# Kernel tuning notes

Hardware: AMD Instinct MI355X
Metric: run time of the kernel (lower is better)

## Reference

```python
import jax, jax.numpy as jnp
import numpy as np


def setup_inputs() -> dict:
    key = jax.random.key(0)
    ks = jax.random.split(key, 7)
    C, IC, H, W, B = 512, 256, 64, 64, 8
    N = H * W
    return {
        "x": jax.random.normal(ks[0], (B, C, H, W), dtype=jnp.float32),
        "w_phi": jax.random.normal(ks[1], (IC, C), dtype=jnp.float32) * 0.02,
        "w_theta": jax.random.normal(ks[2], (IC, C), dtype=jnp.float32) * 0.02,
        "w_g": jax.random.normal(ks[3], (IC, C), dtype=jnp.float32) * 0.02,
        "w_mask": jax.random.normal(ks[4], (C, IC), dtype=jnp.float32) * 0.02,
        "pos_embedding": jax.random.normal(ks[5], (1, N, N), dtype=jnp.float32),
        "pos_embedding_decoder": jax.random.normal(ks[6], (1, IC, H, W), dtype=jnp.float32),
    }


def reference(x, w_phi, w_theta, w_g, w_mask, pos_embedding, pos_embedding_decoder):
    b, c, h, w = x.shape
    n = h * w
    xf = x.reshape(b, c, n)  # [b, c, n]
    # 1x1 convs as channel matmuls
    phi = jnp.einsum('oc,bcn->bon', w_phi, xf)      # [b, ic, n]
    theta = jnp.einsum('oc,bcn->bon', w_theta, xf)  # [b, ic, n]
    g = jnp.einsum('oc,bcn->bon', w_g, xf) + pos_embedding_decoder.reshape(1, -1, n)
    g = jnp.swapaxes(g, 1, 2)  # [b, n, ic]
    # attention logits: theta^T @ phi -> [b, n_theta, n_phi], plus learned pos bias
    attn = jnp.einsum('bci,bcj->bij', theta, phi) + pos_embedding
    # NOTE: original softmax is over dim=1 (the theta/query axis), non-standard
    attn = jax.nn.softmax(attn, axis=1)
    y = jnp.einsum('bij,bjc->bic', attn, g)  # [b, n, ic]
    y = jnp.swapaxes(y, 1, 2).reshape(b, -1, n)  # [b, ic, n]
    mask = jnp.einsum('oc,bcn->bon', w_mask, y).reshape(b, c, h, w)
    return mask + x
```

## Files before the change

kernel.cpp:

```cpp
#include <hip/hip_runtime.h>

typedef short bf8 __attribute__((ext_vector_type(8)));
typedef float f32x4 __attribute__((ext_vector_type(4)));
typedef unsigned short us4 __attribute__((ext_vector_type(4)));
typedef unsigned short us8 __attribute__((ext_vector_type(8)));

#define DEVI __device__ __forceinline__

constexpr int NB = 8, NC = 512, NIC = 256, NS = 4096;

constexpr size_t OFF_XT  = 0;
constexpr size_t OFF_TP  = 33554432;
constexpr size_t OFF_POS = 67108864;
constexpr size_t OFF_G   = 100663296;
constexpr size_t OFF_RS  = 117440512;
constexpr size_t OFF_Y   = 134217728;
constexpr size_t OFF_WTP = 150994944;
constexpr size_t OFF_WG  = 151519232;
constexpr size_t OFF_WM  = 151781376;
constexpr size_t OFF_SP  = 152043520;

DEVI unsigned short f2bf(float f){
  unsigned u = __float_as_uint(f);
  u += 0x7fffu + ((u >> 16) & 1u);
  return (unsigned short)(u >> 16);
}
DEVI float bf2f(unsigned short b){ return __uint_as_float(((unsigned)b) << 16); }

DEVI void gld16(const void* g, void* l){
  __builtin_amdgcn_global_load_lds((const __attribute__((address_space(1))) unsigned int*)g,
                                   (__attribute__((address_space(3))) unsigned int*)l, 16, 0, 0);
}

DEVI void stageT(unsigned short* dst, const unsigned short* src, int ld, int wid, int lane){
  int rl = lane >> 3;
  int ce = ((lane & 7) << 3) ^ (rl << 3);
#pragma unroll
  for (int it = 0; it < 4; ++it){
    int q = wid + it * 4;
    gld16(src + (size_t)(q * 8 + rl) * ld + ce, dst + q * 512);
  }
}

DEVI void zero44(f32x4 (&a)[4][4]){
  f32x4 z = {0.f, 0.f, 0.f, 0.f};
#pragma unroll
  for (int i = 0; i < 4; ++i)
#pragma unroll
    for (int j = 0; j < 4; ++j) a[i][j] = z;
}

template<int NK64>
DEVI void gemm128v(const unsigned short* Ag, int lda, const unsigned short* Bg, int ldb,
                   unsigned short (&As)[2][8192], unsigned short (&Bs)[2][8192],
                   f32x4 (&acc)[4][4], int wid, int lane)
{
  const int wr = wid >> 1, wc = wid & 1;
  stageT(As[0], Ag, lda, wid, lane);
  stageT(Bs[0], Bg, ldb, wid, lane);
  __syncthreads();
  for (int kt = 0; kt < NK64; ++kt){
    int cur = kt & 1;
    if (kt + 1 < NK64){
      stageT(As[cur ^ 1], Ag + (kt + 1) * 64, lda, wid, lane);
      stageT(Bs[cur ^ 1], Bg + (kt + 1) * 64, ldb, wid, lane);
    }
    bf8 a[2][4], b[2][4];
#pragma unroll
    for (int ks = 0; ks < 2; ++ks){
      int cb = ks * 64 + ((lane >> 4) << 4);
#pragma unroll
      for (int f = 0; f < 4; ++f){
        int rA = wr * 64 + f * 16 + (lane & 15);
        a[ks][f] = *(const bf8*)((char*)As[cur] + rA * 128 + (cb ^ ((rA & 7) << 4)));
        int rB = wc * 64 + f * 16 + (lane & 15);
        b[ks][f] = *(const bf8*)((char*)Bs[cur] + rB * 128 + (cb ^ ((rB & 7) << 4)));
      }
    }
    __builtin_amdgcn_s_setprio(1);
#pragma unroll
    for (int ks = 0; ks < 2; ++ks)
#pragma unroll
      for (int i = 0; i < 4; ++i)
#pragma unroll
        for (int j = 0; j < 4; ++j)
          acc[i][j] = __builtin_amdgcn_mfma_f32_16x16x32_bf16(a[ks][i], b[ks][j], acc[i][j], 0, 0, 0);
    __builtin_amdgcn_s_setprio(0);
    __syncthreads();
  }
}


__global__ void k_prep(const float* wphi, const float* wtheta, const float* wgf, const float* wmf,
                       unsigned short* wtp, unsigned short* wgb, unsigned short* wmb){
  int idx = (blockIdx.x * 256 + threadIdx.x) * 4;
  const float* src; unsigned short* dst;
  if (idx < 131072)      { src = wphi + idx;            dst = wtp + idx; }
  else if (idx < 262144) { src = wtheta + (idx - 131072); dst = wtp + idx; }
  else if (idx < 393216) { src = wgf + (idx - 262144);  dst = wgb + (idx - 262144); }
  else                   { src = wmf + (idx - 393216);  dst = wmb + (idx - 393216); }
  f32x4 v = *(const f32x4*)src;
  us4 o;
#pragma unroll
  for (int r = 0; r < 4; ++r) o[r] = f2bf(v[r]);
  *(us4*)dst = o;
}

__global__ void k_pos(const float* pos, unsigned short* posb){
  size_t base = ((size_t)blockIdx.x * 256 + threadIdx.x) * 8;
  f32x4 v0 = *(const f32x4*)&pos[base];
  f32x4 v1 = *(const f32x4*)&pos[base + 4];
  us8 o;
#pragma unroll
  for (int r = 0; r < 4; ++r){ o[r] = f2bf(v0[r]); o[r + 4] = f2bf(v1[r]); }
  *(us8*)&posb[base] = o;
}

__global__ void k_xt(const float* x, unsigned short* xT){
  int b = blockIdx.z, ct = blockIdx.y, nt = blockIdx.x;
  __shared__ float t[64][65];
  int tid = threadIdx.x;
  int c0 = ct * 64, n0 = nt * 64;
  const float* xp = x + (size_t)b * NC * NS;
#pragma unroll
  for (int it = 0; it < 16; ++it){
    int idx = it * 256 + tid; int r = idx >> 6, cc = idx & 63;
    t[r][cc] = xp[(size_t)(c0 + r) * NS + n0 + cc];
  }
  __syncthreads();
  unsigned short* xo = xT + (size_t)b * NS * NC;
#pragma unroll
  for (int it = 0; it < 16; ++it){
    int idx = it * 256 + tid; int r = idx >> 6, cc = idx & 63;
    xo[(size_t)(n0 + r) * NC + c0 + cc] = f2bf(t[cc][r]);
  }
}


__global__ __launch_bounds__(256, 2) void k_tp(const unsigned short* wtp, const unsigned short* xT,
                                               unsigned short* tp){
  int b = blockIdx.z, ot = blockIdx.y, nt = blockIdx.x;
  int tid = threadIdx.x, wid = tid >> 6, lane = tid & 63, wr = wid >> 1, wc = wid & 1;
  __shared__ unsigned short As[2][8192], Bs[2][8192];
  f32x4 acc[4][4]; zero44(acc);
  gemm128v<8>(wtp + (size_t)(ot * 128) * 512, 512,
              xT + ((size_t)b * NS + nt * 128) * 512, 512, As, Bs, acc, wid, lane);
  unsigned short* out = tp + (size_t)b * NS * 512;
#pragma unroll
  for (int fr = 0; fr < 4; ++fr)
#pragma unroll
    for (int fc = 0; fc < 4; ++fc){
      int o0 = ot * 128 + wr * 64 + fr * 16 + ((lane >> 4) << 2);
      int n  = nt * 128 + wc * 64 + fc * 16 + (lane & 15);
      us4 v;
#pragma unroll
      for (int r = 0; r < 4; ++r) v[r] = f2bf(acc[fr][fc][r]);
      *(us4*)&out[(size_t)n * 512 + o0] = v;
    }
}

__global__ __launch_bounds__(256, 2) void k_g(const unsigned short* xT, const unsigned short* wgb,
                                              const float* pdec, unsigned short* gb){
  int b = blockIdx.z, ot = blockIdx.y, nt = blockIdx.x;
  int tid = threadIdx.x, wid = tid >> 6, lane = tid & 63, wr = wid >> 1, wc = wid & 1;
  __shared__ unsigned short As[2][8192], Bs[2][8192];
  f32x4 acc[4][4]; zero44(acc);
  gemm128v<8>(xT + ((size_t)b * NS + nt * 128) * 512, 512,
              wgb + (size_t)(ot * 128) * 512, 512, As, Bs, acc, wid, lane);
#pragma unroll
  for (int fr = 0; fr < 4; ++fr)
#pragma unroll
    for (int fc = 0; fc < 4; ++fc){
      int n0 = nt * 128 + wr * 64 + fr * 16 + ((lane >> 4) << 2);
      int o  = ot * 128 + wc * 64 + fc * 16 + (lane & 15);
      f32x4 pd = *(const f32x4*)&pdec[(size_t)o * NS + n0];
      us4 v;
#pragma unroll
      for (int r = 0; r < 4; ++r) v[r] = f2bf(acc[fr][fc][r] + pd[r]);
      *(us4*)&gb[((size_t)b * NIC + o) * NS + n0] = v;
    }
}

__global__ __launch_bounds__(256, 2) void k_stats(const unsigned short* tp, const unsigned short* posb,
                                                  float* sp){
  int b = blockIdx.z, ih = blockIdx.y, jt = blockIdx.x;
  int tid = threadIdx.x, wid = tid >> 6, lane = tid & 63, wr = wid >> 1, wc = wid & 1;
  __shared__ unsigned short As[2][8192], Bs[2][8192];
  __shared__ float sred[2][2][64];
  float sacc[4][4];
#pragma unroll
  for (int i = 0; i < 4; ++i)
#pragma unroll
    for (int j = 0; j < 4; ++j) sacc[i][j] = 0.f;
  const unsigned short* tpb = tp + (size_t)b * NS * 512;
  const unsigned short* Ag = tpb + (size_t)(jt * 128) * 512;
  for (int it8 = 0; it8 < 8; ++it8){
    int i0 = (ih * 8 + it8) * 128;
    const unsigned short* Bg = tpb + (size_t)i0 * 512 + 256;
    f32x4 acc[4][4]; zero44(acc);
    gemm128v<4>(Ag, 512, Bg, 512, As, Bs, acc, wid, lane);
#pragma unroll
    for (int fr = 0; fr < 4; ++fr)
#pragma unroll
      for (int fc = 0; fc < 4; ++fc){
        int ig  = i0 + wc * 64 + fc * 16 + (lane & 15);
        int jg0 = jt * 128 + wr * 64 + fr * 16 + ((lane >> 4) << 2);
        us4 pv = *(const us4*)&posb[(size_t)ig * NS + jg0];
#pragma unroll
        for (int r = 0; r < 4; ++r)
          sacc[fr][r] += __expf(acc[fr][fc][r] + bf2f(pv[r]));
      }
  }
#pragma unroll
  for (int m = 1; m <= 8; m <<= 1)
#pragma unroll
    for (int fr = 0; fr < 4; ++fr)
#pragma unroll
      for (int r = 0; r < 4; ++r)
        sacc[fr][r] += __shfl_xor(sacc[fr][r], m, 64);
  if ((lane & 15) == 0){
#pragma unroll
    for (int fr = 0; fr < 4; ++fr)
#pragma unroll
      for (int r = 0; r < 4; ++r)
        sred[wr][wc][fr * 16 + ((lane >> 4) << 2) + r] = sacc[fr][r];
  }
  __syncthreads();
  if (tid < 128){
    int jl = tid;
    sp[((size_t)b * 4 + ih) * NS + jt * 128 + jl] = sred[jl >> 6][0][jl & 63] + sred[jl >> 6][1][jl & 63];
  }
}

__global__ void k_rs(const float* sp, float* rs){
  int idx = blockIdx.x * 256 + threadIdx.x;
  int b = idx >> 12, j = idx & 4095;
  const float* spb = sp + (size_t)b * 4 * NS + j;
  rs[idx] = 1.f / (spb[0] + spb[NS] + spb[2 * NS] + spb[3 * NS]);
}

__global__ __launch_bounds__(256, 2) void k_y(const unsigned short* tp, const unsigned short* posb,
                                              const unsigned short* gb, const float* rs,
                                              unsigned short* yb){
  int b = blockIdx.y, i0 = blockIdx.x * 64;
  int tid = threadIdx.x, wid = tid >> 6, lane = tid & 63;
  __shared__ unsigned short Th[64 * 256];
  __shared__ unsigned short Aph[2][128 * 64];
  __shared__ unsigned short El[64 * 128];
  const unsigned short* tpb = tp + (size_t)b * NS * 512;

#pragma unroll
  for (int t = 0; t < 8; ++t){
    int cid = t * 256 + tid;
    int row = cid >> 5, ch = cid & 31;
    int dstb = row * 512 + ((ch * 16) ^ ((row & 7) << 4));
    *(us8*)((char*)Th + dstb) = *(const us8*)&tpb[(size_t)(i0 + row) * 512 + 256 + ch * 8];
  }
  f32x4 yacc[4][4]; zero44(yacc);
  stageT(Aph[0], tpb, 512, wid, lane);
  __syncthreads();

  const unsigned short* gbb = gb + (size_t)b * NIC * NS;
  const float* rsb = rs + (size_t)b * NS;

  for (int jt = 0; jt < 32; ++jt){
    int j0 = jt * 128;
    const unsigned short* phiBase = tpb + (size_t)j0 * 512;
    f32x4 lacc[2][4];
    {
      f32x4 z = {0.f, 0.f, 0.f, 0.f};
#pragma unroll
      for (int i = 0; i < 2; ++i)
#pragma unroll
        for (int j = 0; j < 4; ++j) lacc[i][j] = z;
    }
#pragma unroll
    for (int ph = 0; ph < 4; ++ph){
      int cur = ph & 1;
      if (ph < 3) stageT(Aph[cur ^ 1], phiBase + (ph + 1) * 64, 512, wid, lane);
      bf8 a[2][2], bt[2][4];
#pragma unroll
      for (int ks = 0; ks < 2; ++ks){
#pragma unroll
        for (int f = 0; f < 2; ++f){
          int r = wid * 32 + f * 16 + (lane & 15);
          int lb = ks * 64 + ((lane >> 4) << 4);
          a[ks][f] = *(const bf8*)((char*)Aph[cur] + r * 128 + (lb ^ ((r & 7) << 4)));
        }
#pragma unroll
        for (int f = 0; f < 4; ++f){
          int ti = f * 16 + (lane & 15);
          int tb = ph * 128 + ks * 64 + ((lane >> 4) << 4);
          bt[ks][f] = *(const bf8*)((char*)Th + ti * 512 + (tb ^ ((ti & 7) << 4)));
        }
      }
      __builtin_amdgcn_s_setprio(1);
#pragma unroll
      for (int ks = 0; ks < 2; ++ks)
#pragma unroll
        for (int fr = 0; fr < 2; ++fr)
#pragma unroll
          for (int fc = 0; fc < 4; ++fc)
            lacc[fr][fc] = __builtin_amdgcn_mfma_f32_16x16x32_bf16(a[ks][fr], bt[ks][fc], lacc[fr][fc], 0, 0, 0);
      __builtin_amdgcn_s_setprio(0);
      if (ph < 3) __syncthreads();
    }
#pragma unroll
    for (int fr = 0; fr < 2; ++fr)
#pragma unroll
      for (int fc = 0; fc < 4; ++fc){
        int il = fc * 16 + (lane & 15);
        int jl = wid * 32 + fr * 16 + ((lane >> 4) << 2);
        us4 pv = *(const us4*)&posb[(size_t)(i0 + il) * NS + j0 + jl];
        f32x4 rv = *(const f32x4*)&rsb[j0 + jl];
        us4 ev;
#pragma unroll
        for (int r = 0; r < 4; ++r)
          ev[r] = f2bf(__expf(lacc[fr][fc][r] + bf2f(pv[r])) * rv[r]);
        *(us4*)((char*)El + il * 256 + ((jl * 2) ^ ((il & 7) << 4))) = ev;
      }
    __syncthreads();
    if (jt < 31) stageT(Aph[0], tpb + (size_t)(j0 + 128) * 512, 512, wid, lane);
#pragma unroll
    for (int jk = 0; jk < 4; ++jk){
      bf8 eb[4];
#pragma unroll
      for (int f = 0; f < 4; ++f){
        int ei = f * 16 + (lane & 15);
        int ebt = jk * 64 + ((lane >> 4) << 4);
        eb[f] = *(const bf8*)((char*)El + ei * 256 + (ebt ^ ((ei & 7) << 4)));
      }
      __builtin_amdgcn_s_setprio(1);
#pragma unroll
      for (int cf = 0; cf < 4; ++cf){
        int c = wid * 64 + cf * 16 + (lane & 15);
        bf8 ga = *(const bf8*)&gbb[(size_t)c * NS + j0 + jk * 32 + (lane >> 4) * 8];
#pragma unroll
        for (int f = 0; f < 4; ++f)
          yacc[cf][f] = __builtin_amdgcn_mfma_f32_16x16x32_bf16(ga, eb[f], yacc[cf][f], 0, 0, 0);
      }
      __builtin_amdgcn_s_setprio(0);
    }
    __syncthreads();
  }
  unsigned short* yo = yb + (size_t)b * NS * NIC;
#pragma unroll
  for (int cf = 0; cf < 4; ++cf)
#pragma unroll
    for (int f = 0; f < 4; ++f){
      int c0 = wid * 64 + cf * 16 + ((lane >> 4) << 2);
      int ig = i0 + f * 16 + (lane & 15);
      us4 v;
#pragma unroll
      for (int r = 0; r < 4; ++r) v[r] = f2bf(yacc[cf][f][r]);
      *(us4*)&yo[(size_t)ig * NIC + c0] = v;
    }
}

__global__ __launch_bounds__(256, 2) void k_out(const unsigned short* yb, const unsigned short* wmb,
                                                const float* xg, float* outg){
  int b = blockIdx.z, cot = blockIdx.y, nt = blockIdx.x;
  int tid = threadIdx.x, wid = tid >> 6, lane = tid & 63, wr = wid >> 1, wc = wid & 1;
  __shared__ unsigned short As[2][8192], Bs[2][8192];
  f32x4 acc[4][4]; zero44(acc);
  gemm128v<4>(yb + ((size_t)b * NS + nt * 128) * 256, 256,
              wmb + (size_t)(cot * 128) * 256, 256, As, Bs, acc, wid, lane);
#pragma unroll
  for (int fr = 0; fr < 4; ++fr)
#pragma unroll
    for (int fc = 0; fc < 4; ++fc){
      int n0 = nt * 128 + wr * 64 + fr * 16 + ((lane >> 4) << 2);
      int co = cot * 128 + wc * 64 + fc * 16 + (lane & 15);
      f32x4 xv = *(const f32x4*)&xg[((size_t)b * NC + co) * NS + n0];
      f32x4 ov = acc[fr][fc] + xv;
      *(f32x4*)&outg[((size_t)b * NC + co) * NS + n0] = ov;
    }
}

extern "C" void kernel_launch(void* const* d_in, const int* in_sizes, int n_in,
                              void* d_out, int out_size, void* d_ws, size_t ws_size,
                              hipStream_t stream){
  const float* x      = (const float*)d_in[0];
  const float* wphi   = (const float*)d_in[1];
  const float* wtheta = (const float*)d_in[2];
  const float* wgf    = (const float*)d_in[3];
  const float* wmf    = (const float*)d_in[4];
  const float* pos    = (const float*)d_in[5];
  const float* pdec   = (const float*)d_in[6];
  float* outg = (float*)d_out;
  char* ws = (char*)d_ws;
  unsigned short* xT   = (unsigned short*)(ws + OFF_XT);
  unsigned short* tp   = (unsigned short*)(ws + OFF_TP);
  unsigned short* posb = (unsigned short*)(ws + OFF_POS);
  unsigned short* gb   = (unsigned short*)(ws + OFF_G);
  float*          rsv  = (float*)(ws + OFF_RS);
  unsigned short* yb   = (unsigned short*)(ws + OFF_Y);
  unsigned short* wtp  = (unsigned short*)(ws + OFF_WTP);
  unsigned short* wgb  = (unsigned short*)(ws + OFF_WG);
  unsigned short* wmb  = (unsigned short*)(ws + OFF_WM);
  float* sp = (float*)(ws + OFF_SP);

  k_prep<<<512, 256, 0, stream>>>(wphi, wtheta, wgf, wmf, wtp, wgb, wmb);
  k_pos<<<8192, 256, 0, stream>>>(pos, posb);
  k_xt<<<dim3(64, 8, 8), 256, 0, stream>>>(x, xT);
  k_tp<<<dim3(32, 4, 8), 256, 0, stream>>>(wtp, xT, tp);
  k_g<<<dim3(32, 2, 8), 256, 0, stream>>>(xT, wgb, pdec, gb);
  k_stats<<<dim3(32, 4, 8), 256, 0, stream>>>(tp, posb, sp);
  k_rs<<<128, 256, 0, stream>>>(sp, rsv);
  k_y<<<dim3(64, 8), 256, 0, stream>>>(tp, posb, gb, rsv, yb);
  k_out<<<dim3(32, 4, 8), 256, 0, stream>>>(yb, wmb, x, outg);
}
```

Measured before the change: 515.2 us.

## Prescale g by softmax reciprocals and restructure k_y with register theta and 4-stage phi pipeline

A new k_sg kernel folds the softmax column reciprocal into g ahead of time, so k_y no longer multiplies by rs per logit. k_y keeps each wave's theta fragments in registers instead of LDS and uses a 2x2 wave split for the logit tile. It adds a 4-deep LDS ring for phi with a manual vmcnt wait and raw barriers, and prefetches the pos tile before the MFMA loop. The trailing __syncthreads is also removed. The cost is an extra full pass over g, higher register pressure, and rs aliased onto the xT buffer, plus tricky hand-written synchronisation that is easy to get wrong.

```diff
diff --git a/kernel.cpp b/kernel.cpp
--- a/kernel.cpp
+++ b/kernel.cpp
@@ -10,10 +10,11 @@
 constexpr int NB = 8, NC = 512, NIC = 256, NS = 4096;
 
 constexpr size_t OFF_XT  = 0;
+constexpr size_t OFF_RS  = 0;
 constexpr size_t OFF_TP  = 33554432;
 constexpr size_t OFF_POS = 67108864;
 constexpr size_t OFF_G   = 100663296;
-constexpr size_t OFF_RS  = 117440512;
+constexpr size_t OFF_G2  = 117440512;
 constexpr size_t OFF_Y   = 134217728;
 constexpr size_t OFF_WTP = 150994944;
 constexpr size_t OFF_WG  = 151519232;
@@ -239,88 +240,112 @@
   rs[idx] = 1.f / (spb[0] + spb[NS] + spb[2 * NS] + spb[3 * NS]);
 }
 
-__global__ __launch_bounds__(256, 2) void k_y(const unsigned short* tp, const unsigned short* posb,
-                                              const unsigned short* gb, const float* rs,
-                                              unsigned short* yb){
+__global__ void k_sg(const unsigned short* gb, const float* rs, unsigned short* g2){
+  size_t base = ((size_t)blockIdx.x * 256 + threadIdx.x) * 8;
+  int b = (int)(base / ((size_t)NIC * NS));
+  int j0 = (int)(base % NS);
+  const float* rsb = rs + (size_t)b * NS + j0;
+  f32x4 r0 = *(const f32x4*)&rsb[0];
+  f32x4 r1 = *(const f32x4*)&rsb[4];
+  us8 gv = *(const us8*)&gb[base];
+  us8 o;
+#pragma unroll
+  for (int r = 0; r < 4; ++r){
+    o[r]     = f2bf(bf2f(gv[r])     * r0[r]);
+    o[r + 4] = f2bf(bf2f(gv[r + 4]) * r1[r]);
+  }
+  *(us8*)&g2[base] = o;
+}
+
+__global__ __launch_bounds__(256, 2) void k_y(const unsigned short* __restrict__ tp,
+                                              const unsigned short* __restrict__ posb,
+                                              const unsigned short* __restrict__ g2,
+                                              unsigned short* __restrict__ yb){
   int b = blockIdx.y, i0 = blockIdx.x * 64;
   int tid = threadIdx.x, wid = tid >> 6, lane = tid & 63;
-  __shared__ unsigned short Th[64 * 256];
-  __shared__ unsigned short Aph[2][128 * 64];
+  int p = wid >> 1, q = wid & 1;
+  __shared__ unsigned short Aph[4][128 * 64];
   __shared__ unsigned short El[64 * 128];
   const unsigned short* tpb = tp + (size_t)b * NS * 512;
 
-#pragma unroll
-  for (int t = 0; t < 8; ++t){
-    int cid = t * 256 + tid;
-    int row = cid >> 5, ch = cid & 31;
-    int dstb = row * 512 + ((ch * 16) ^ ((row & 7) << 4));
-    *(us8*)((char*)Th + dstb) = *(const us8*)&tpb[(size_t)(i0 + row) * 512 + 256 + ch * 8];
-  }
+  bf8 btr[8][2];
+#pragma unroll
+  for (int kb = 0; kb < 8; ++kb)
+#pragma unroll
+    for (int fc = 0; fc < 2; ++fc)
+      btr[kb][fc] = *(const bf8*)&tpb[(size_t)(i0 + p * 32 + fc * 16 + (lane & 15)) * 512
+                                      + 256 + kb * 32 + (lane >> 4) * 8];
+
   f32x4 yacc[4][4]; zero44(yacc);
   stageT(Aph[0], tpb, 512, wid, lane);
-  __syncthreads();
-
-  const unsigned short* gbb = gb + (size_t)b * NIC * NS;
-  const float* rsb = rs + (size_t)b * NS;
+  stageT(Aph[1], tpb + 64, 512, wid, lane);
+
+  const unsigned short* g2b = g2 + (size_t)b * NIC * NS;
 
   for (int jt = 0; jt < 32; ++jt){
     int j0 = jt * 128;
     const unsigned short* phiBase = tpb + (size_t)j0 * 512;
-    f32x4 lacc[2][4];
+    const unsigned short* phiNext = tpb + (size_t)(jt < 31 ? j0 + 128 : j0) * 512;
+    us4 pv[4][2];
+#pragma unroll
+    for (int fr = 0; fr < 4; ++fr){
+      int jl = q * 64 + fr * 16 + ((lane >> 4) << 2);
+#pragma unroll
+      for (int fc = 0; fc < 2; ++fc){
+        int il = p * 32 + fc * 16 + (lane & 15);
+        pv[fr][fc] = *(const us4*)&posb[(size_t)(i0 + il) * NS + j0 + jl];
+      }
+    }
+    f32x4 lacc[4][2];
     {
       f32x4 z = {0.f, 0.f, 0.f, 0.f};
 #pragma unroll
-      for (int i = 0; i < 2; ++i)
-#pragma unroll
-        for (int j = 0; j < 4; ++j) lacc[i][j] = z;
+      for (int i = 0; i < 4; ++i)
+#pragma unroll
+        for (int j = 0; j < 2; ++j) lacc[i][j] = z;
     }
 #pragma unroll
     for (int ph = 0; ph < 4; ++ph){
-      int cur = ph & 1;
-      if (ph < 3) stageT(Aph[cur ^ 1], phiBase + (ph + 1) * 64, 512, wid, lane);
-      bf8 a[2][2], bt[2][4];
+      const unsigned short* ssrc = (ph < 2) ? phiBase + (ph + 2) * 64 : phiNext + (ph - 2) * 64;
+      stageT(Aph[(ph + 2) & 3], ssrc, 512, wid, lane);
+      asm volatile("s_waitcnt vmcnt(32)" ::: "memory");
+      __builtin_amdgcn_s_barrier();
+      __builtin_amdgcn_sched_barrier(0);
 #pragma unroll
       for (int ks = 0; ks < 2; ++ks){
-#pragma unroll
-        for (int f = 0; f < 2; ++f){
-          int r = wid * 32 + f * 16 + (lane & 15);
-          int lb = ks * 64 + ((lane >> 4) << 4);
-          a[ks][f] = *(const bf8*)((char*)Aph[cur] + r * 128 + (lb ^ ((r & 7) << 4)));
+        bf8 a[4];
+#pragma unroll
+        for (int fr = 0; fr < 4; ++fr){
+          int r = q * 64 + fr * 16 + (lane & 15);
+          int cbyte = (ks * 64 + ((lane >> 4) << 4)) ^ ((r & 7) << 4);
+          a[fr] = *(const bf8*)((char*)Aph[ph] + r * 128 + cbyte);
         }
-#pragma unroll
-        for (int f = 0; f < 4; ++f){
-          int ti = f * 16 + (lane & 15);
-          int tb = ph * 128 + ks * 64 + ((lane >> 4) << 4);
-          bt[ks][f] = *(const bf8*)((char*)Th + ti * 512 + (tb ^ ((ti & 7) << 4)));
-        }
-      }
-      __builtin_amdgcn_s_setprio(1);
-#pragma unroll
-      for (int ks = 0; ks < 2; ++ks)
-#pragma unroll
-        for (int fr = 0; fr < 2; ++fr)
-#pragma unroll
-          for (int fc = 0; fc < 4; ++fc)
-            lacc[fr][fc] = __builtin_amdgcn_mfma_f32_16x16x32_bf16(a[ks][fr], bt[ks][fc], lacc[fr][fc], 0, 0, 0);
-      __builtin_amdgcn_s_setprio(0);
-      if (ph < 3) __syncthreads();
-    }
-#pragma unroll
-    for (int fr = 0; fr < 2; ++fr)
-#pragma unroll
-      for (int fc = 0; fc < 4; ++fc){
-        int il = fc * 16 + (lane & 15);
-        int jl = wid * 32 + fr * 16 + ((lane >> 4) << 2);
-        us4 pv = *(const us4*)&posb[(size_t)(i0 + il) * NS + j0 + jl];
-        f32x4 rv = *(const f32x4*)&rsb[j0 + jl];
+        __builtin_amdgcn_s_setprio(1);
+#pragma unroll
+        for (int fr = 0; fr < 4; ++fr)
+#pragma unroll
+          for (int fc = 0; fc < 2; ++fc)
+            lacc[fr][fc] = __builtin_amdgcn_mfma_f32_16x16x32_bf16(a[fr], btr[ph * 2 + ks][fc],
+                                                                   lacc[fr][fc], 0, 0, 0);
+        __builtin_amdgcn_s_setprio(0);
+      }
+    }
+#pragma unroll
+    for (int fr = 0; fr < 4; ++fr)
+#pragma unroll
+      for (int fc = 0; fc < 2; ++fc){
+        int il = p * 32 + fc * 16 + (lane & 15);
+        int jl = q * 64 + fr * 16 + ((lane >> 4) << 2);
         us4 ev;
 #pragma unroll
         for (int r = 0; r < 4; ++r)
-          ev[r] = f2bf(__expf(lacc[fr][fc][r] + bf2f(pv[r])) * rv[r]);
+          ev[r] = f2bf(__expf(lacc[fr][fc][r] + bf2f(pv[fr][fc][r])));
         *(us4*)((char*)El + il * 256 + ((jl * 2) ^ ((il & 7) << 4))) = ev;
       }
-    __syncthreads();
-    if (jt < 31) stageT(Aph[0], tpb + (size_t)(j0 + 128) * 512, 512, wid, lane);
+    __builtin_amdgcn_sched_barrier(0);
+    asm volatile("s_waitcnt lgkmcnt(0)" ::: "memory");
+    __builtin_amdgcn_s_barrier();
+    __builtin_amdgcn_sched_barrier(0);
 #pragma unroll
     for (int jk = 0; jk < 4; ++jk){
       bf8 eb[4];
@@ -334,14 +359,13 @@
 #pragma unroll
       for (int cf = 0; cf < 4; ++cf){
         int c = wid * 64 + cf * 16 + (lane & 15);
-        bf8 ga = *(const bf8*)&gbb[(size_t)c * NS + j0 + jk * 32 + (lane >> 4) * 8];
+        bf8 ga = *(const bf8*)&g2b[(size_t)c * NS + j0 + jk * 32 + (lane >> 4) * 8];
 #pragma unroll
         for (int f = 0; f < 4; ++f)
           yacc[cf][f] = __builtin_amdgcn_mfma_f32_16x16x32_bf16(ga, eb[f], yacc[cf][f], 0, 0, 0);
       }
       __builtin_amdgcn_s_setprio(0);
     }
-    __syncthreads();
   }
   unsigned short* yo = yb + (size_t)b * NS * NIC;
 #pragma unroll
@@ -390,10 +414,11 @@
   float* outg = (float*)d_out;
   char* ws = (char*)d_ws;
   unsigned short* xT   = (unsigned short*)(ws + OFF_XT);
+  float*          rsv  = (float*)(ws + OFF_RS);
   unsigned short* tp   = (unsigned short*)(ws + OFF_TP);
   unsigned short* posb = (unsigned short*)(ws + OFF_POS);
   unsigned short* gb   = (unsigned short*)(ws + OFF_G);
-  float*          rsv  = (float*)(ws + OFF_RS);
+  unsigned short* g2   = (unsigned short*)(ws + OFF_G2);
   unsigned short* yb   = (unsigned short*)(ws + OFF_Y);
   unsigned short* wtp  = (unsigned short*)(ws + OFF_WTP);
   unsigned short* wgb  = (unsigned short*)(ws + OFF_WG);
@@ -407,6 +432,7 @@
   k_g<<<dim3(32, 2, 8), 256, 0, stream>>>(xT, wgb, pdec, gb);
   k_stats<<<dim3(32, 4, 8), 256, 0, stream>>>(tp, posb, sp);
   k_rs<<<128, 256, 0, stream>>>(sp, rsv);
-  k_y<<<dim3(64, 8), 256, 0, stream>>>(tp, posb, gb, rsv, yb);
+  k_sg<<<4096, 256, 0, stream>>>(gb, rsv, g2);
+  k_y<<<dim3(64, 8), 256, 0, stream>>>(tp, posb, g2, yb);
   k_out<<<dim3(32, 4, 8), 256, 0, stream>>>(yb, wmb, x, outg);
 }
```

After: 487.2 us. 5.4% less time.
